# Optimization experiments

Measured on AMD Instinct MI355X. Metric: run time of the kernel, lower is better.

## Reference

```python
import jax, jax.numpy as jnp
import numpy as np

H1, H2, IN, LAT = 64, 32, 2, 16

def _lstm(x, Wih, Whh, bih, bhh, H):
    # x: [B, T, I]; gate order i,f,g,o (PyTorch convention)
    B, T, _ = x.shape
    xg = jnp.einsum('bti,gi->btg', x, Wih) + bih + bhh  # [B, T, 4H]
    xg = jnp.transpose(xg, (1, 0, 2))  # [T, B, 4H]

    def step(carry, xg_t):
        h, c = carry
        gates = xg_t + h @ Whh.T
        i, f, g, o = jnp.split(gates, 4, axis=-1)
        i = jax.nn.sigmoid(i); f = jax.nn.sigmoid(f)
        g = jnp.tanh(g); o = jax.nn.sigmoid(o)
        c = f * c + i * g
        h = o * jnp.tanh(c)
        return (h, c), h

    h0 = jnp.zeros((B, H), x.dtype)
    c0 = jnp.zeros((B, H), x.dtype)
    (h_last, _), hs = jax.lax.scan(step, (h0, c0), xg)
    return jnp.transpose(hs, (1, 0, 2)), h_last  # [B,T,H], [B,H]


def setup_inputs() -> dict:
    key = jax.random.key(0)
    ks = jax.random.split(key, 12)
    s = 0.1
    return {
        'x': jax.random.normal(ks[0], (512, 4096, IN), jnp.float32),
        'Wih1': jax.random.normal(ks[1], (4 * H1, IN), jnp.float32) * s,
        'Whh1': jax.random.normal(ks[2], (4 * H1, H1), jnp.float32) * s,
        'bih1': jax.random.normal(ks[3], (4 * H1,), jnp.float32) * s,
        'bhh1': jax.random.normal(ks[4], (4 * H1,), jnp.float32) * s,
        'Wih2': jax.random.normal(ks[5], (4 * H2, H1), jnp.float32) * s,
        'Whh2': jax.random.normal(ks[6], (4 * H2, H2), jnp.float32) * s,
        'bih2': jax.random.normal(ks[7], (4 * H2,), jnp.float32) * s,
        'bhh2': jax.random.normal(ks[8], (4 * H2,), jnp.float32) * s,
        'Wfc': jax.random.normal(ks[9], (LAT, H2), jnp.float32) * s,
        'bfc': jax.random.normal(ks[10], (LAT,), jnp.float32) * s,
    }


def reference(x, Wih1, Whh1, bih1, bhh1, Wih2, Whh2, bih2, bhh2, Wfc, bfc):
    h1_seq, _ = _lstm(x, Wih1, Whh1, bih1, bhh1, H1)      # [B,T,64]
    _, h2_last = _lstm(h1_seq, Wih2, Whh2, bih2, bhh2, H2)  # [B,32] == x[:, -1, :]
    return h2_last @ Wfc.T + bfc  # [B,16]
```

## Files before the change

kernel.cpp:

```cpp
#include <hip/hip_runtime.h>


#define TT 4096
#define BB 512
#define NCH 64

typedef float    f4  __attribute__((ext_vector_type(4)));
typedef int      i4  __attribute__((ext_vector_type(4)));
typedef _Float16 h2v __attribute__((ext_vector_type(2)));
typedef _Float16 h8  __attribute__((ext_vector_type(8)));

__device__ __forceinline__ float fexp2(float x){ return __builtin_amdgcn_exp2f(x); }
__device__ __forceinline__ float frcp (float x){ return __builtin_amdgcn_rcpf(x); }
__device__ __forceinline__ float lgs  (float p){ return frcp(1.0f + fexp2(p)); }
__device__ __forceinline__ float tanh_(float x){ return 1.0f - 2.0f * frcp(1.0f + fexp2(x * 2.8853900817779268f)); }

#define BARRIER() asm volatile("s_waitcnt lgkmcnt(0)\n\ts_barrier" ::: "memory")

__device__ __forceinline__ h2v bch(int s){ return __builtin_bit_cast(h2v, s); }
__device__ __forceinline__ float dot8(h8 a, i4 bi, float c){
  const i4 ai = __builtin_bit_cast(i4, a);
  c = __builtin_amdgcn_fdot2(bch(ai.x), bch(bi.x), c, false);
  c = __builtin_amdgcn_fdot2(bch(ai.y), bch(bi.y), c, false);
  c = __builtin_amdgcn_fdot2(bch(ai.z), bch(bi.z), c, false);
  c = __builtin_amdgcn_fdot2(bch(ai.w), bch(bi.w), c, false);
  return c;
}
__device__ __forceinline__ float fdh(int a, int b, float c){
  return __builtin_amdgcn_fdot2(bch(a), bch(b), c, false);
}
__device__ __forceinline__ int pack16(float a, float b){
  h2v p; p.x = (_Float16)a; p.y = (_Float16)b;
  return __builtin_bit_cast(int, p);
}
__device__ __forceinline__ h8 ldh8s(const float* p, float s){
  const f4 a = ((const f4*)p)[0], b = ((const f4*)p)[1];
  h8 r;
  r[0]=(_Float16)(a.x*s); r[1]=(_Float16)(a.y*s); r[2]=(_Float16)(a.z*s); r[3]=(_Float16)(a.w*s);
  r[4]=(_Float16)(b.x*s); r[5]=(_Float16)(b.y*s); r[6]=(_Float16)(b.z*s); r[7]=(_Float16)(b.w*s);
  return r;
}

extern "C" __global__ __launch_bounds__(256, 1) void lstm_enc_kernel(
    const float* __restrict__ x,
    const float* __restrict__ Wih1, const float* __restrict__ Whh1,
    const float* __restrict__ bih1, const float* __restrict__ bhh1,
    const float* __restrict__ Wih2, const float* __restrict__ Whh2,
    const float* __restrict__ bih2, const float* __restrict__ bhh2,
    const float* __restrict__ Wfc,  const float* __restrict__ bfc,
    float* __restrict__ out)
{
    const int tid = threadIdx.x;
    const int l   = tid & 63;
    const int wv  = __builtin_amdgcn_readfirstlane(tid >> 6);
    const int be  = wv >> 1;
    const bool isL1 = ((wv & 1) == 0);
    const int bg  = blockIdx.x * 2 + be;

    __shared__ __align__(16) _Float16 ring[2][128][64];
    __shared__ __align__(16) _Float16 h2r[2][2][32];
    __shared__ int xs[2][2][64];

    const float kSs = -1.4426950408889634f;
    const float kSg = -2.8853900817779268f;

    if (isL1) {
        h8 wi[8], wf[8], wg[8], wo[8];
        const int ri = l, rf = 64 + l, rg = 128 + l, ro = 192 + l;
        #pragma unroll
        for (int j = 0; j < 8; ++j) {
            wi[j] = ldh8s(Whh1 + ri*64 + j*8, kSs);
            wf[j] = ldh8s(Whh1 + rf*64 + j*8, kSs);
            wg[j] = ldh8s(Whh1 + rg*64 + j*8, kSg);
            wo[j] = ldh8s(Whh1 + ro*64 + j*8, kSs);
        }
        const int wxi = pack16(Wih1[ri*2]*kSs, Wih1[ri*2+1]*kSs);
        const int wxf = pack16(Wih1[rf*2]*kSs, Wih1[rf*2+1]*kSs);
        const int wxg = pack16(Wih1[rg*2]*kSg, Wih1[rg*2+1]*kSg);
        const int wxo = pack16(Wih1[ro*2]*kSs, Wih1[ro*2+1]*kSs);
        const float bi_ = (bih1[ri] + bhh1[ri]) * kSs;
        const float bf_ = (bih1[rf] + bhh1[rf]) * kSs;
        const float bg_ = (bih1[rg] + bhh1[rg]) * kSg;
        const float bo_ = (bih1[ro] + bhh1[ro]) * kSs;

        if (l < 32) ((int*)&ring[be][127][0])[l] = 0;
        BARRIER();

        float cc = 0.f;
        _Float16* rw = &ring[be][0][0];
        const i4* rd = (const i4*)&ring[be][0][0];

#define L1S(PR, CR, XV) { \
    const i4* Hp = rd + (PR)*8; \
    i4 H[8]; \
    _Pragma("unroll") for (int j = 0; j < 8; ++j) H[j] = Hp[j]; \
    float ai = bi_, af = bf_, ag = bg_, ao = bo_; \
    _Pragma("unroll") for (int j = 0; j < 8; ++j) { \
        ai = dot8(wi[j], H[j], ai); af = dot8(wf[j], H[j], af); \
        ag = dot8(wg[j], H[j], ag); ao = dot8(wo[j], H[j], ao); } \
    const int xv_ = (XV); \
    ai = fdh(wxi, xv_, ai); af = fdh(wxf, xv_, af); \
    ag = fdh(wxg, xv_, ag); ao = fdh(wxo, xv_, ao); \
    const float gi = lgs(ai), gf = lgs(af), go = lgs(ao); \
    const float gg = fmaf(2.f, lgs(ag), -1.f); \
    cc = fmaf(gf, cc, gi * gg); \
    rw[(CR)*64 + l] = (_Float16)(go * tanh_(cc)); }

        #pragma unroll 1
        for (int c = 0; c <= NCH; ++c) {
            if (c < NCH) {
                const int base = (c & 1) * 64;
                const int p0 = (base ^ 64) + 63;
                const int* xc = xs[be][c & 1];
                L1S(p0, base, xc[0])
                #pragma unroll 2
                for (int s = 1; s < 64; ++s) { L1S(base + s - 1, base + s, xc[s]) }
            }
            BARRIER();
        }
#undef L1S
    } else {
        const int u = l & 31, hf = l >> 5;
        const float hff = (float)hf;
        const int rA = hf * 64 + u;
        const int rB = hf * 64 + 32 + u;
        const float kA = hf ? kSg : kSs;
        h8 wa[12], wb[12];
        #pragma unroll
        for (int j = 0; j < 8; ++j) {
            wa[j] = ldh8s(Wih2 + rA*64 + j*8, kA);
            wb[j] = ldh8s(Wih2 + rB*64 + j*8, kSs);
        }
        #pragma unroll
        for (int j = 0; j < 4; ++j) {
            wa[8+j] = ldh8s(Whh2 + rA*32 + j*8, kA);
            wb[8+j] = ldh8s(Whh2 + rB*32 + j*8, kSs);
        }
        const float ba_ = (bih2[rA] + bhh2[rA]) * kA;
        const float bb_ = (bih2[rB] + bhh2[rB]) * kSs;

        if (l < 16) ((int*)&h2r[be][1][0])[l] = 0;
        const float2* xb2 = (const float2*)(x + (size_t)bg * (TT * 2));
        {
            const float2 c0 = xb2[l];
            xs[be][0][l] = pack16(c0.x, c0.y);
        }
        float2 vxn = xb2[64 + l];
        BARRIER();

        float c2 = 0.f;
        const i4* rdh = (const i4*)&ring[be][0][0];
        const i4* g0 = (const i4*)&h2r[be][0][0];
        const i4* g1 = (const i4*)&h2r[be][1][0];
        _Float16* q0 = &h2r[be][0][0];
        _Float16* q1 = &h2r[be][1][0];

#define L2S(S, GR, QW) { \
    const i4* Hp = rc + (S)*8; \
    i4 H[8]; \
    _Pragma("unroll") for (int j = 0; j < 8; ++j) H[j] = Hp[j]; \
    i4 G[4]; \
    _Pragma("unroll") for (int j = 0; j < 4; ++j) G[j] = (GR)[j]; \
    float pa = ba_, pb = bb_; \
    _Pragma("unroll") for (int j = 0; j < 8; ++j) { \
        pa = dot8(wa[j], H[j], pa); pb = dot8(wb[j], H[j], pb); } \
    _Pragma("unroll") for (int j = 0; j < 4; ++j) { \
        pa = dot8(wa[8+j], G[j], pa); pb = dot8(wb[8+j], G[j], pb); } \
    const float sa = lgs(pa); \
    const float va = fmaf(hff, sa - 1.f, sa);    \
    const float vb = lgs(pb);                    \
    const float oa = __shfl_xor(va, 32); \
    const float ob = __shfl_xor(vb, 32); \
    const float gi = hf ? oa : va, gf = hf ? ob : vb; \
    const float gg = hf ? va : oa, go = hf ? vb : ob; \
    c2 = fmaf(gf, c2, gi * gg); \
    const float h2n = go * tanh_(c2); \
    if (!hf) (QW)[u] = (_Float16)h2n; }

        #pragma unroll 1
        for (int c = 0; c <= NCH; ++c) {
            if (c + 1 < NCH) xs[be][(c + 1) & 1][l] = pack16(vxn.x, vxn.y);
            if (c + 2 < NCH) vxn = xb2[(c + 2) * 64 + l];
            if (c > 0) {
                const i4* rc = rdh + ((c - 1) & 1) * 64 * 8;
                for (int s = 0; s < 64; s += 2) {
                    L2S(s,     g1, q0)
                    L2S(s + 1, g0, q1)
                }
            }
            BARRIER();
        }
#undef L2S

        if (l < 16) {
            float sum = bfc[l];
            const float* wr = Wfc + l * 32;
            #pragma unroll
            for (int k = 0; k < 32; ++k) sum = fmaf(wr[k], (float)h2r[be][1][k], sum);
            out[bg * 16 + l] = sum;
        }
    }
}

extern "C" void kernel_launch(void* const* d_in, const int* in_sizes, int n_in,
                              void* d_out, int out_size, void* d_ws, size_t ws_size,
                              hipStream_t stream) {
    const float* x    = (const float*)d_in[0];
    const float* Wih1 = (const float*)d_in[1];
    const float* Whh1 = (const float*)d_in[2];
    const float* bih1 = (const float*)d_in[3];
    const float* bhh1 = (const float*)d_in[4];
    const float* Wih2 = (const float*)d_in[5];
    const float* Whh2 = (const float*)d_in[6];
    const float* bih2 = (const float*)d_in[7];
    const float* bhh2 = (const float*)d_in[8];
    const float* Wfc  = (const float*)d_in[9];
    const float* bfc  = (const float*)d_in[10];

    hipLaunchKernelGGL(lstm_enc_kernel, dim3(BB / 2), dim3(256), 0, stream,
        x, Wih1, Whh1, bih1, bhh1, Wih2, Whh2, bih2, bhh2, Wfc, bfc,
        (float*)d_out);
}
```

Baseline: 1.556 ms.

## Fuse both LSTM layers into one wavefront per batch, software-pipelined without barriers

Before, each batch element used two wavefronts, one per layer, handing off 64-step chunks through LDS with workgroup barriers. Now a single 64-lane wavefront per batch element holds both layers' weights in registers. It interleaves layer-1 step s of chunk c with layer-2 step s of chunk c-1 in the same instruction stream, so no barriers are needed and the two recurrences give each other independent work for latency hiding. The risks are very high register pressure, which could cause spills, and serialising both layers' arithmetic onto one wave instead of running them concurrently on two.

```diff
diff --git a/kernel.cpp b/kernel.cpp
--- a/kernel.cpp
+++ b/kernel.cpp
@@ -14,8 +14,6 @@
 __device__ __forceinline__ float frcp (float x){ return __builtin_amdgcn_rcpf(x); }
 __device__ __forceinline__ float lgs  (float p){ return frcp(1.0f + fexp2(p)); }
 __device__ __forceinline__ float tanh_(float x){ return 1.0f - 2.0f * frcp(1.0f + fexp2(x * 2.8853900817779268f)); }
-
-#define BARRIER() asm volatile("s_waitcnt lgkmcnt(0)\n\ts_barrier" ::: "memory")
 
 __device__ __forceinline__ h2v bch(int s){ return __builtin_bit_cast(h2v, s); }
 __device__ __forceinline__ float dot8(h8 a, i4 bi, float c){
@@ -41,7 +39,7 @@
   return r;
 }
 
-extern "C" __global__ __launch_bounds__(256, 1) void lstm_enc_kernel(
+extern "C" __global__ __launch_bounds__(64, 1) void lstm_enc_kernel(
     const float* __restrict__ x,
     const float* __restrict__ Wih1, const float* __restrict__ Whh1,
     const float* __restrict__ bih1, const float* __restrict__ bhh1,
@@ -50,45 +48,71 @@
     const float* __restrict__ Wfc,  const float* __restrict__ bfc,
     float* __restrict__ out)
 {
-    const int tid = threadIdx.x;
-    const int l   = tid & 63;
-    const int wv  = __builtin_amdgcn_readfirstlane(tid >> 6);
-    const int be  = wv >> 1;
-    const bool isL1 = ((wv & 1) == 0);
-    const int bg  = blockIdx.x * 2 + be;
-
-    __shared__ __align__(16) _Float16 ring[2][128][64];
-    __shared__ __align__(16) _Float16 h2r[2][2][32];
-    __shared__ int xs[2][2][64];
+    const int l = threadIdx.x;
+    const int b = blockIdx.x;
+
+    __shared__ __align__(16) _Float16 ring[128][64];
+    __shared__ __align__(16) _Float16 h2r[2][32];
+    __shared__ int xs[2][64];
 
     const float kSs = -1.4426950408889634f;
     const float kSg = -2.8853900817779268f;
 
-    if (isL1) {
-        h8 wi[8], wf[8], wg[8], wo[8];
-        const int ri = l, rf = 64 + l, rg = 128 + l, ro = 192 + l;
-        #pragma unroll
-        for (int j = 0; j < 8; ++j) {
-            wi[j] = ldh8s(Whh1 + ri*64 + j*8, kSs);
-            wf[j] = ldh8s(Whh1 + rf*64 + j*8, kSs);
-            wg[j] = ldh8s(Whh1 + rg*64 + j*8, kSg);
-            wo[j] = ldh8s(Whh1 + ro*64 + j*8, kSs);
-        }
-        const int wxi = pack16(Wih1[ri*2]*kSs, Wih1[ri*2+1]*kSs);
-        const int wxf = pack16(Wih1[rf*2]*kSs, Wih1[rf*2+1]*kSs);
-        const int wxg = pack16(Wih1[rg*2]*kSg, Wih1[rg*2+1]*kSg);
-        const int wxo = pack16(Wih1[ro*2]*kSs, Wih1[ro*2+1]*kSs);
-        const float bi_ = (bih1[ri] + bhh1[ri]) * kSs;
-        const float bf_ = (bih1[rf] + bhh1[rf]) * kSs;
-        const float bg_ = (bih1[rg] + bhh1[rg]) * kSg;
-        const float bo_ = (bih1[ro] + bhh1[ro]) * kSs;
-
-        if (l < 32) ((int*)&ring[be][127][0])[l] = 0;
-        BARRIER();
-
-        float cc = 0.f;
-        _Float16* rw = &ring[be][0][0];
-        const i4* rd = (const i4*)&ring[be][0][0];
+    const int ri = l, rf = 64 + l, rg = 128 + l, ro = 192 + l;
+    h8 wi[8], wf[8], wg[8], wo[8];
+    #pragma unroll
+    for (int j = 0; j < 8; ++j) {
+        wi[j] = ldh8s(Whh1 + ri*64 + j*8, kSs);
+        wf[j] = ldh8s(Whh1 + rf*64 + j*8, kSs);
+        wg[j] = ldh8s(Whh1 + rg*64 + j*8, kSg);
+        wo[j] = ldh8s(Whh1 + ro*64 + j*8, kSs);
+    }
+    const int wxi = pack16(Wih1[ri*2]*kSs, Wih1[ri*2+1]*kSs);
+    const int wxf = pack16(Wih1[rf*2]*kSs, Wih1[rf*2+1]*kSs);
+    const int wxg = pack16(Wih1[rg*2]*kSg, Wih1[rg*2+1]*kSg);
+    const int wxo = pack16(Wih1[ro*2]*kSs, Wih1[ro*2+1]*kSs);
+    const float bi_ = (bih1[ri] + bhh1[ri]) * kSs;
+    const float bf_ = (bih1[rf] + bhh1[rf]) * kSs;
+    const float bg_ = (bih1[rg] + bhh1[rg]) * kSg;
+    const float bo_ = (bih1[ro] + bhh1[ro]) * kSs;
+
+    const int u = l & 31, hf = l >> 5;
+    const float hff = (float)hf;
+    const int rA = hf * 64 + u;
+    const int rB = hf * 64 + 32 + u;
+    const float kA = hf ? kSg : kSs;
+    h8 wa[12], wb[12];
+    #pragma unroll
+    for (int j = 0; j < 8; ++j) {
+        wa[j] = ldh8s(Wih2 + rA*64 + j*8, kA);
+        wb[j] = ldh8s(Wih2 + rB*64 + j*8, kSs);
+    }
+    #pragma unroll
+    for (int j = 0; j < 4; ++j) {
+        wa[8+j] = ldh8s(Whh2 + rA*32 + j*8, kA);
+        wb[8+j] = ldh8s(Whh2 + rB*32 + j*8, kSs);
+    }
+    const float ba_ = (bih2[rA] + bhh2[rA]) * kA;
+    const float bb_ = (bih2[rB] + bhh2[rB]) * kSs;
+
+    if (l < 32) ((int*)&ring[127][0])[l] = 0;
+    if (l < 16) ((int*)&h2r[1][0])[l] = 0;
+    const float2* xb2 = (const float2*)(x + (size_t)b * (TT * 2));
+    {
+        const float2 c0 = xb2[l];
+        xs[0][l] = pack16(c0.x, c0.y);
+    }
+    float2 vxn = xb2[64 + l];
+
+    float cc = 0.f;
+    float c2 = 0.f;
+
+    const i4* rd = (const i4*)&ring[0][0];
+    _Float16* rw = &ring[0][0];
+    const i4* g0 = (const i4*)&h2r[0][0];
+    const i4* g1 = (const i4*)&h2r[1][0];
+    _Float16* q0 = &h2r[0][0];
+    _Float16* q1 = &h2r[1][0];
 
 #define L1S(PR, CR, XV) { \
     const i4* Hp = rd + (PR)*8; \
@@ -106,57 +130,8 @@
     cc = fmaf(gf, cc, gi * gg); \
     rw[(CR)*64 + l] = (_Float16)(go * tanh_(cc)); }
 
-        #pragma unroll 1
-        for (int c = 0; c <= NCH; ++c) {
-            if (c < NCH) {
-                const int base = (c & 1) * 64;
-                const int p0 = (base ^ 64) + 63;
-                const int* xc = xs[be][c & 1];
-                L1S(p0, base, xc[0])
-                #pragma unroll 2
-                for (int s = 1; s < 64; ++s) { L1S(base + s - 1, base + s, xc[s]) }
-            }
-            BARRIER();
-        }
-#undef L1S
-    } else {
-        const int u = l & 31, hf = l >> 5;
-        const float hff = (float)hf;
-        const int rA = hf * 64 + u;
-        const int rB = hf * 64 + 32 + u;
-        const float kA = hf ? kSg : kSs;
-        h8 wa[12], wb[12];
-        #pragma unroll
-        for (int j = 0; j < 8; ++j) {
-            wa[j] = ldh8s(Wih2 + rA*64 + j*8, kA);
-            wb[j] = ldh8s(Wih2 + rB*64 + j*8, kSs);
-        }
-        #pragma unroll
-        for (int j = 0; j < 4; ++j) {
-            wa[8+j] = ldh8s(Whh2 + rA*32 + j*8, kA);
-            wb[8+j] = ldh8s(Whh2 + rB*32 + j*8, kSs);
-        }
-        const float ba_ = (bih2[rA] + bhh2[rA]) * kA;
-        const float bb_ = (bih2[rB] + bhh2[rB]) * kSs;
-
-        if (l < 16) ((int*)&h2r[be][1][0])[l] = 0;
-        const float2* xb2 = (const float2*)(x + (size_t)bg * (TT * 2));
-        {
-            const float2 c0 = xb2[l];
-            xs[be][0][l] = pack16(c0.x, c0.y);
-        }
-        float2 vxn = xb2[64 + l];
-        BARRIER();
-
-        float c2 = 0.f;
-        const i4* rdh = (const i4*)&ring[be][0][0];
-        const i4* g0 = (const i4*)&h2r[be][0][0];
-        const i4* g1 = (const i4*)&h2r[be][1][0];
-        _Float16* q0 = &h2r[be][0][0];
-        _Float16* q1 = &h2r[be][1][0];
-
-#define L2S(S, GR, QW) { \
-    const i4* Hp = rc + (S)*8; \
+#define L2S(RR, GR, QW) { \
+    const i4* Hp = rd + (RR)*8; \
     i4 H[8]; \
     _Pragma("unroll") for (int j = 0; j < 8; ++j) H[j] = Hp[j]; \
     i4 G[4]; \
@@ -171,34 +146,53 @@
     const float vb = lgs(pb);                    \
     const float oa = __shfl_xor(va, 32); \
     const float ob = __shfl_xor(vb, 32); \
-    const float gi = hf ? oa : va, gf = hf ? ob : vb; \
-    const float gg = hf ? va : oa, go = hf ? vb : ob; \
-    c2 = fmaf(gf, c2, gi * gg); \
-    const float h2n = go * tanh_(c2); \
+    const float gi2 = hf ? oa : va, gf2 = hf ? ob : vb; \
+    const float gg2 = hf ? va : oa, go2 = hf ? vb : ob; \
+    c2 = fmaf(gf2, c2, gi2 * gg2); \
+    const float h2n = go2 * tanh_(c2); \
     if (!hf) (QW)[u] = (_Float16)h2n; }
 
+    {
+        const int* xc = xs[0];
         #pragma unroll 1
-        for (int c = 0; c <= NCH; ++c) {
-            if (c + 1 < NCH) xs[be][(c + 1) & 1][l] = pack16(vxn.x, vxn.y);
-            if (c + 2 < NCH) vxn = xb2[(c + 2) * 64 + l];
-            if (c > 0) {
-                const i4* rc = rdh + ((c - 1) & 1) * 64 * 8;
-                for (int s = 0; s < 64; s += 2) {
-                    L2S(s,     g1, q0)
-                    L2S(s + 1, g0, q1)
-                }
-            }
-            BARRIER();
+        for (int s = 0; s < 64; s += 2) {
+            L1S((s + 127) & 127, s,     xc[s])
+            L1S(s,               s + 1, xc[s + 1])
         }
+    }
+
+    #pragma unroll 1
+    for (int c = 1; c < NCH; ++c) {
+        xs[c & 1][l] = pack16(vxn.x, vxn.y);
+        if (c + 1 < NCH) vxn = xb2[(c + 1) * 64 + l];
+        const int* xc = xs[c & 1];
+        const int b1 = (c & 1) << 6;
+        const int b2 = b1 ^ 64;
+        #pragma unroll 1
+        for (int s = 0; s < 64; s += 2) {
+            L1S((b1 + s + 127) & 127, b1 + s,     xc[s])
+            L2S(b2 + s,     g1, q0)
+            L1S(b1 + s,               b1 + s + 1, xc[s + 1])
+            L2S(b2 + s + 1, g0, q1)
+        }
+    }
+
+    {
+        #pragma unroll 1
+        for (int s = 0; s < 64; s += 2) {
+            L2S(64 + s,     g1, q0)
+            L2S(64 + s + 1, g0, q1)
+        }
+    }
+#undef L1S
 #undef L2S
 
-        if (l < 16) {
-            float sum = bfc[l];
-            const float* wr = Wfc + l * 32;
-            #pragma unroll
-            for (int k = 0; k < 32; ++k) sum = fmaf(wr[k], (float)h2r[be][1][k], sum);
-            out[bg * 16 + l] = sum;
-        }
+    if (l < 16) {
+        float sum = bfc[l];
+        const float* wr = Wfc + l * 32;
+        #pragma unroll
+        for (int k = 0; k < 32; ++k) sum = fmaf(wr[k], (float)h2r[1][k], sum);
+        out[b * 16 + l] = sum;
     }
 }
 
@@ -217,7 +211,7 @@
     const float* Wfc  = (const float*)d_in[9];
     const float* bfc  = (const float*)d_in[10];
 
-    hipLaunchKernelGGL(lstm_enc_kernel, dim3(BB / 2), dim3(256), 0, stream,
+    hipLaunchKernelGGL(lstm_enc_kernel, dim3(BB), dim3(64), 0, stream,
         x, Wih1, Whh1, bih1, bhh1, Wih2, Whh2, bih2, bhh2, Wfc, bfc,
         (float*)d_out);
 }
```

After: 5.037 ms. +223.6%, slower.
